# Performance work log

Measured on AMD Instinct MI355X. Metric: run time of the kernel, lower is better.

## Reference

```python
import jax, jax.numpy as jnp
import numpy as np

N = 100000
E = 3200000
H = 16


def setup_inputs() -> dict:
    key = jax.random.key(0)
    ks = jax.random.split(key, 8)
    x = jax.random.normal(ks[0], (N, 1), dtype=jnp.float32)
    edge_index = jax.random.randint(ks[1], (2, E), 0, N, dtype=jnp.int64)
    # GCNConv weights (PyG: lin has no bias by default? it has bias=True via separate bias param)
    W1 = jax.random.normal(ks[2], (1, H), dtype=jnp.float32) / np.sqrt(1.0)
    b1 = jnp.zeros((H,), dtype=jnp.float32)
    W2 = jax.random.normal(ks[3], (H, H), dtype=jnp.float32) / np.sqrt(H)
    b2 = jnp.zeros((H,), dtype=jnp.float32)
    Wf = jax.random.normal(ks[4], (H, 1), dtype=jnp.float32) / np.sqrt(H)
    bf = jnp.zeros((1,), dtype=jnp.float32)
    return {"x": x, "edge_index": edge_index, "W1": W1, "b1": b1,
            "W2": W2, "b2": b2, "Wf": Wf, "bf": bf}


def _gcn_norm(edge_index, num_nodes):
    # add self-loops, compute symmetric normalization coeffs per edge
    loops = jnp.arange(num_nodes, dtype=edge_index.dtype)
    src = jnp.concatenate([edge_index[0], loops])
    dst = jnp.concatenate([edge_index[1], loops])
    deg = jax.ops.segment_sum(jnp.ones_like(dst, dtype=jnp.float32), dst,
                              num_segments=num_nodes)
    dinv = jnp.where(deg > 0, jax.lax.rsqrt(deg), 0.0)
    norm = dinv[src] * dinv[dst]  # [E+N]
    return src, dst, norm


def _gcn_conv(h, src, dst, norm, W, b, num_nodes):
    h = h @ W                              # [N, out]
    msg = h[src] * norm[:, None]           # gather + scale, [E+N, out]
    agg = jax.ops.segment_sum(msg, dst, num_segments=num_nodes)
    return agg + b


def reference(x, edge_index, W1, b1, W2, b2, Wf, bf):
    num_nodes = x.shape[0]
    src, dst, norm = _gcn_norm(edge_index, num_nodes)
    h = _gcn_conv(x, src, dst, norm, W1, b1, num_nodes)
    h = jax.nn.relu(h)
    h = _gcn_conv(h, src, dst, norm, W2, b2, num_nodes)
    h = jax.nn.relu(h)
    out = jnp.tanh(h @ Wf + bf)            # [N, 1]
    return out
```

## Files before the change

### kernel.cpp

```cpp
#include <hip/hip_runtime.h>
#include <hip/hip_fp16.h>
#include <math.h>

#define HID 16
typedef unsigned int uint;

#define PSHIFT 7
#define PSIZE  128
#define PMASK  127
#define SRCBITS 17
#define SRCMASK 0x1FFFFu
#define SENT 0xFFFFFFFFu
#define PAD 16
#define TILE 8192
#define MAXNB 1024
#define AGT 1024
#define CAP 6144


__global__ void p_bcount(const int* __restrict__ dstA, uint* __restrict__ tileHist,
                         int e, int nb) {
    __shared__ uint hist[MAXNB];
    int t = threadIdx.x;
    for (int i = t; i < nb; i += 256) hist[i] = 0;
    __syncthreads();
    int base = blockIdx.x * TILE;
    int lim = min(TILE, e - base);
    const int4* d4 = (const int4*)(dstA + base);
    int n4 = lim >> 2;
    for (int k = t; k < n4; k += 256) {
        int4 d = d4[k];
        atomicAdd(&hist[((uint)d.x) >> PSHIFT], 1u);
        atomicAdd(&hist[((uint)d.y) >> PSHIFT], 1u);
        atomicAdd(&hist[((uint)d.z) >> PSHIFT], 1u);
        atomicAdd(&hist[((uint)d.w) >> PSHIFT], 1u);
    }
    for (int i = (n4 << 2) + t; i < lim; i += 256)
        atomicAdd(&hist[((uint)dstA[base + i]) >> PSHIFT], 1u);
    __syncthreads();
    size_t row = (size_t)blockIdx.x * nb;
    for (int i = t; i < nb; i += 256)
        tileHist[row + i] = hist[i];
}

__global__ void p_colsum(const uint* __restrict__ tileHist, uint* __restrict__ bCnt,
                         int tiles, int nb) {
    __shared__ uint red[256];
    int b = blockIdx.x;
    int t = threadIdx.x;
    uint s = 0;
    for (int ti = t; ti < tiles; ti += 256)
        s += tileHist[(size_t)ti * nb + b];
    red[t] = s;
    __syncthreads();
    for (int off = 128; off >= 1; off >>= 1) {
        if (t < off) red[t] += red[t + off];
        __syncthreads();
    }
    if (t == 0) bCnt[b] = red[0];
}

__global__ void p_bscan(const uint* __restrict__ bCnt, uint* __restrict__ cursorPad,
                        uint* __restrict__ bBase, int nb) {
    __shared__ uint tsum[256];
    int t = threadIdx.x;
    uint loc[4]; uint s = 0;
#pragma unroll
    for (int k = 0; k < 4; ++k) {
        int i = t * 4 + k;
        uint c = (i < nb) ? bCnt[i] : 0u;
        loc[k] = s; s += c;
    }
    tsum[t] = s;
    __syncthreads();
    for (int off = 1; off < 256; off <<= 1) {
        uint v = (t >= off) ? tsum[t - off] : 0u;
        __syncthreads();
        tsum[t] += v;
        __syncthreads();
    }
    uint excl = (t == 0) ? 0u : tsum[t - 1];
#pragma unroll
    for (int k = 0; k < 4; ++k) {
        int i = t * 4 + k;
        if (i < nb) {
            uint b = excl + loc[k];
            bBase[i] = b;
            cursorPad[i * PAD] = b;
        }
    }
}

__global__ void p_part(const int* __restrict__ srcA, const int* __restrict__ dstA,
                       uint* __restrict__ cursorPad, const uint* __restrict__ tileHist,
                       uint* __restrict__ part, int e, int nb) {
    __shared__ uint payload[TILE];
    __shared__ uint hist[MAXNB];
    __shared__ uint binStart[MAXNB];
    __shared__ uint cursorL[MAXNB];
    __shared__ uint gdelta[MAXNB];
    __shared__ uint tsum[256];
    int t = threadIdx.x;
    size_t row = (size_t)blockIdx.x * nb;
    for (int i = t; i < nb; i += 256) hist[i] = tileHist[row + i];
    __syncthreads();
    int base = blockIdx.x * TILE;
    int lim = min(TILE, e - base);
    const int4* s4 = (const int4*)(srcA + base);
    const int4* d4 = (const int4*)(dstA + base);
    int n4 = lim >> 2;
    uint loc[4]; uint s = 0;
#pragma unroll
    for (int k = 0; k < 4; ++k) {
        int i = t * 4 + k;
        uint c = (i < nb) ? hist[i] : 0u;
        loc[k] = s; s += c;
    }
    tsum[t] = s;
    __syncthreads();
    for (int off = 1; off < 256; off <<= 1) {
        uint v = (t >= off) ? tsum[t - off] : 0u;
        __syncthreads();
        tsum[t] += v;
        __syncthreads();
    }
    uint excl = (t == 0) ? 0u : tsum[t - 1];
#pragma unroll
    for (int k = 0; k < 4; ++k) {
        int i = t * 4 + k;
        if (i < nb) {
            uint bs = excl + loc[k];
            binStart[i] = bs; cursorL[i] = bs;
            uint c = hist[i];
            if (c) gdelta[i] = atomicAdd(&cursorPad[i * PAD], c) - bs;
        }
    }
    __syncthreads();
    for (int k = t; k < n4; k += 256) {
        int4 dd = d4[k]; int4 ss = s4[k];
#pragma unroll
        for (int q = 0; q < 4; ++q) {
            uint d = (uint)((q == 0) ? dd.x : (q == 1) ? dd.y : (q == 2) ? dd.z : dd.w);
            uint sv = (uint)((q == 0) ? ss.x : (q == 1) ? ss.y : (q == 2) ? ss.z : ss.w);
            uint w = ((d & PMASK) << SRCBITS) | sv;
            uint pos = atomicAdd(&cursorL[d >> PSHIFT], 1u);
            payload[pos] = w;
        }
    }
    for (int i = (n4 << 2) + t; i < lim; i += 256) {
        uint d = (uint)dstA[base + i];
        uint w = ((d & PMASK) << SRCBITS) | (uint)srcA[base + i];
        uint pos = atomicAdd(&cursorL[d >> PSHIFT], 1u);
        payload[pos] = w;
    }
    __syncthreads();
    int grp = t >> 4, lane16 = t & 15;
    for (int bk = grp; bk < nb; bk += 16) {
        uint c = hist[bk];
        if (!c) continue;
        uint st = binStart[bk];
        uint gd = gdelta[bk];
        for (uint i = lane16; i < c; i += 16)
            part[gd + st + i] = payload[st + i];
    }
}

__global__ __launch_bounds__(AGT)
void p_sort(uint* __restrict__ part, const uint* __restrict__ bBase,
            const uint* __restrict__ bCnt, const float* __restrict__ x,
            uint* __restrict__ rowEnd, uint* __restrict__ oversz,
            float* __restrict__ dinv, float* __restrict__ y, int n) {
    __shared__ uint lds[2 * CAP];
    __shared__ uint hist[PSIZE];
    __shared__ uint cursor[PSIZE];
    int b = blockIdx.x, t = threadIdx.x;
    uint base = bBase[b], cnt = bCnt[b];
    if (t < PSIZE) hist[t] = 0;
    if (t == 0) oversz[b] = (cnt > 2 * CAP) ? 1u : 0u;
    __syncthreads();
    bool fits = (cnt <= 2 * CAP);
    if (fits) {
        for (uint i = t; i < cnt; i += AGT) {
            uint w = part[base + i];
            lds[i] = w;
            atomicAdd(&hist[w >> SRCBITS], 1u);
        }
    } else {
        for (uint i = t; i < cnt; i += AGT)
            atomicAdd(&hist[part[base + i] >> SRCBITS], 1u);
    }
    __syncthreads();
    uint myc = (t < PSIZE) ? hist[t] : 0u;
    for (int off = 1; off < PSIZE; off <<= 1) {
        uint v = 0;
        if (t < PSIZE && t >= off) v = hist[t - off];
        __syncthreads();
        if (t < PSIZE) hist[t] += v;
        __syncthreads();
    }
    if (t < PSIZE) cursor[t] = hist[t] - myc;
    __syncthreads();
    if (fits) {
        if (cnt <= CAP) {
            for (uint i = t; i < cnt; i += AGT) {
                uint w = lds[i];
                uint pos = atomicAdd(&cursor[w >> SRCBITS], 1u);
                lds[CAP + pos] = w & SRCMASK;
            }
            __syncthreads();
            for (uint i = t; i < cnt; i += AGT)
                part[base + i] = lds[CAP + i];
        } else {
            for (uint i = t; i < cnt; i += AGT) {
                uint w = lds[i];
                uint pos = atomicAdd(&cursor[w >> SRCBITS], 1u);
                part[base + pos] = w & SRCMASK;
            }
        }
    }
    if (t < PSIZE) {
        int node = b * PSIZE + t;
        if (node < n) {
            rowEnd[node] = fits ? (base + hist[t]) : SENT;
            float d = rsqrtf((float)(myc + 1u));
            dinv[node] = d;
            y[node] = x[node] * d;
        }
    }
}

__global__ void p_g1mlp(const uint* __restrict__ part, const uint* __restrict__ rowEnd,
                        const uint* __restrict__ bBase,
                        const float* __restrict__ y, const float* __restrict__ dinv,
                        const float* __restrict__ W1, const float* __restrict__ b1,
                        const float* __restrict__ W2,
                        __half* __restrict__ g, int n) {
    int i = blockIdx.x * blockDim.x + threadIdx.x;
    if (i >= n) return;
    uint en = rowEnd[i];
    if (en == SENT) return;
    uint st = (i & PMASK) ? rowEnd[i - 1] : bBase[i >> PSHIFT];
    float tsum = 0.0f;
    uint e = st;
    for (; e + 4 <= en; e += 4)
        tsum += y[part[e]] + y[part[e + 1]] + y[part[e + 2]] + y[part[e + 3]];
    for (; e < en; ++e) tsum += y[part[e]];
    float d = dinv[i];
    float sv = d * (tsum + y[i]);
    float h1[HID], h2[HID];
#pragma unroll
    for (int j = 0; j < HID; ++j)
        h1[j] = fmaxf(sv * W1[j] + b1[j], 0.0f);
#pragma unroll
    for (int k = 0; k < HID; ++k) {
        float a = 0.0f;
#pragma unroll
        for (int j = 0; j < HID; ++j)
            a = fmaf(h1[j], W2[j * HID + k], a);
        h2[k] = a * d;
    }
    __half2 hh[8];
#pragma unroll
    for (int q = 0; q < 8; ++q)
        hh[q] = __floats2half2_rn(h2[2 * q], h2[2 * q + 1]);
    uint4* gp = (uint4*)(g + (size_t)i * HID);
    gp[0] = *reinterpret_cast<uint4*>(&hh[0]);
    gp[1] = *reinterpret_cast<uint4*>(&hh[4]);
}

__global__ void p_g2out(const uint* __restrict__ part, const uint* __restrict__ rowEnd,
                        const uint* __restrict__ bBase,
                        const __half* __restrict__ g, const float* __restrict__ dinv,
                        const float* __restrict__ b2, const float* __restrict__ Wf,
                        const float* __restrict__ bf,
                        float* __restrict__ out, int n) {
    int gid = blockIdx.x * blockDim.x + threadIdx.x;
    int node = gid >> 3, lane = gid & 7;
    if (node >= n) return;
    uint en = rowEnd[node];
    if (en == SENT) return;
    uint st = (node & PMASK) ? rowEnd[node - 1] : bBase[node >> PSHIFT];
    const __half2* gh = (const __half2*)g;
    float ax = 0.0f, ay = 0.0f;
    uint e = st;
    for (; e + 4 <= en; e += 4) {
        uint s0 = part[e], s1 = part[e + 1], s2 = part[e + 2], s3 = part[e + 3];
        float2 f0 = __half22float2(gh[(size_t)s0 * 8 + lane]);
        float2 f1 = __half22float2(gh[(size_t)s1 * 8 + lane]);
        float2 f2 = __half22float2(gh[(size_t)s2 * 8 + lane]);
        float2 f3 = __half22float2(gh[(size_t)s3 * 8 + lane]);
        ax += (f0.x + f1.x) + (f2.x + f3.x);
        ay += (f0.y + f1.y) + (f2.y + f3.y);
    }
    for (; e < en; ++e) {
        float2 f = __half22float2(gh[(size_t)part[e] * 8 + lane]);
        ax += f.x; ay += f.y;
    }
    float2 fs = __half22float2(gh[(size_t)node * 8 + lane]);
    ax += fs.x; ay += fs.y;
    float d = dinv[node];
    int j0 = 2 * lane, j1 = 2 * lane + 1;
    float h0 = fmaxf(fmaf(d, ax, b2[j0]), 0.0f);
    float h1 = fmaxf(fmaf(d, ay, b2[j1]), 0.0f);
    float v = h0 * Wf[j0] + h1 * Wf[j1];
#pragma unroll
    for (int m = 4; m >= 1; m >>= 1)
        v += __shfl_xor(v, m, 8);
    if (lane == 0) out[node] = tanhf(v + bf[0]);
}

__global__ __launch_bounds__(AGT)
void p_slow1(const uint* __restrict__ part, const uint* __restrict__ bBase,
             const uint* __restrict__ bCnt, const uint* __restrict__ oversz,
             const float* __restrict__ y, const float* __restrict__ dinv,
             const float* __restrict__ W1, const float* __restrict__ b1,
             const float* __restrict__ W2, __half* __restrict__ g, int n) {
    int b = blockIdx.x;
    if (!oversz[b]) return;
    __shared__ float acc[PSIZE];
    int t = threadIdx.x;
    if (t < PSIZE) acc[t] = 0.0f;
    __syncthreads();
    uint base = bBase[b], cnt = bCnt[b];
    for (uint i = base + t; i < base + cnt; i += AGT) {
        uint w = part[i];
        atomicAdd(&acc[w >> SRCBITS], y[w & SRCMASK]);
    }
    __syncthreads();
    if (t < PSIZE) {
        int node = b * PSIZE + t;
        if (node < n) {
            float d = dinv[node];
            float sv = d * (acc[t] + y[node]);
            float h1[HID], h2[HID];
#pragma unroll
            for (int j = 0; j < HID; ++j)
                h1[j] = fmaxf(sv * W1[j] + b1[j], 0.0f);
#pragma unroll
            for (int k = 0; k < HID; ++k) {
                float a = 0.0f;
#pragma unroll
                for (int j = 0; j < HID; ++j)
                    a = fmaf(h1[j], W2[j * HID + k], a);
                h2[k] = a * d;
            }
            __half2 hh[8];
#pragma unroll
            for (int q = 0; q < 8; ++q)
                hh[q] = __floats2half2_rn(h2[2 * q], h2[2 * q + 1]);
            uint4* gp = (uint4*)(g + (size_t)node * HID);
            gp[0] = *reinterpret_cast<uint4*>(&hh[0]);
            gp[1] = *reinterpret_cast<uint4*>(&hh[4]);
        }
    }
}

__global__ __launch_bounds__(AGT)
void p_slow2(const uint* __restrict__ part, const uint* __restrict__ bBase,
             const uint* __restrict__ bCnt, const uint* __restrict__ oversz,
             const __half* __restrict__ g, const float* __restrict__ dinv,
             const float* __restrict__ b2, const float* __restrict__ Wf,
             const float* __restrict__ bf, float* __restrict__ out, int n) {
    int b = blockIdx.x;
    if (!oversz[b]) return;
    __shared__ float acc[PSIZE][HID + 1];
    int t = threadIdx.x;
    const __half2* gh = (const __half2*)g;
    {
        int r = t >> 3, q = t & 7;
        int node = b * PSIZE + r;
        float2 f = make_float2(0.0f, 0.0f);
        if (node < n) f = __half22float2(gh[(size_t)node * 8 + q]);
        acc[r][2 * q] = f.x; acc[r][2 * q + 1] = f.y;
    }
    __syncthreads();
    uint base = bBase[b], cnt = bCnt[b];
    int gi = t >> 3, sub = t & 7;
    for (uint i = base + gi; i < base + cnt; i += AGT / 8) {
        uint w = part[i];
        uint src = w & SRCMASK;
        uint dl = w >> SRCBITS;
        float2 f = __half22float2(gh[(size_t)src * 8 + sub]);
        atomicAdd(&acc[dl][2 * sub], f.x);
        atomicAdd(&acc[dl][2 * sub + 1], f.y);
    }
    __syncthreads();
    if (t < PSIZE) {
        int node = b * PSIZE + t;
        if (node < n) {
            float d = dinv[node];
            float o = bf[0];
#pragma unroll
            for (int j = 0; j < HID; ++j) {
                float h = fmaxf(fmaf(d, acc[t][j], b2[j]), 0.0f);
                o = fmaf(h, Wf[j], o);
            }
            out[node] = tanhf(o);
        }
    }
}


__global__ void f_init_deg(float* deg, int n) {
    int i = blockIdx.x * blockDim.x + threadIdx.x;
    if (i < n) deg[i] = 1.0f;
}

__global__ void f_deg_accum(const int* __restrict__ dstA, float* deg, int e) {
    int i = blockIdx.x * blockDim.x + threadIdx.x;
    if (i < e) atomicAdd(&deg[dstA[i]], 1.0f);
}

__global__ void f_dinv_s(const float* __restrict__ x, float* deg_dinv, float* s, int n) {
    int i = blockIdx.x * blockDim.x + threadIdx.x;
    if (i < n) {
        float d = rsqrtf(deg_dinv[i]);
        deg_dinv[i] = d;
        s[i] = x[i] * d * d;
    }
}

__global__ void f_s_edge(const int* __restrict__ srcA, const int* __restrict__ dstA,
                         const float* __restrict__ x, const float* __restrict__ dinv,
                         float* s, int e) {
    int i = blockIdx.x * blockDim.x + threadIdx.x;
    if (i < e) {
        int si = srcA[i], di = dstA[i];
        atomicAdd(&s[di], x[si] * dinv[si] * dinv[di]);
    }
}

__global__ void f_node_mlp(const float* __restrict__ s, const float* __restrict__ dinv,
                           const float* __restrict__ W1, const float* __restrict__ b1,
                           const float* __restrict__ W2,
                           float* __restrict__ h2pre, float* __restrict__ agg2, int n) {
    int i = blockIdx.x * blockDim.x + threadIdx.x;
    if (i >= n) return;
    float sv = s[i];
    float h1[HID];
#pragma unroll
    for (int j = 0; j < HID; ++j)
        h1[j] = fmaxf(sv * W1[j] + b1[j], 0.0f);
    float d2 = dinv[i] * dinv[i];
    float h2[HID];
#pragma unroll
    for (int k = 0; k < HID; ++k) {
        float acc = 0.0f;
#pragma unroll
        for (int j = 0; j < HID; ++j)
            acc = fmaf(h1[j], W2[j * HID + k], acc);
        h2[k] = acc;
    }
    float4* hp = (float4*)(h2pre + (size_t)i * HID);
    float4* ap = (float4*)(agg2 + (size_t)i * HID);
#pragma unroll
    for (int q = 0; q < 4; ++q) {
        float4 v = make_float4(h2[q*4+0], h2[q*4+1], h2[q*4+2], h2[q*4+3]);
        hp[q] = v;
        ap[q] = make_float4(v.x * d2, v.y * d2, v.z * d2, v.w * d2);
    }
}

__global__ void f_agg_edge(const int* __restrict__ srcA, const int* __restrict__ dstA,
                           const float* __restrict__ dinv,
                           const float* __restrict__ h2pre,
                           float* __restrict__ agg2, int e) {
    int gid = blockIdx.x * blockDim.x + threadIdx.x;
    int ei = gid >> 4;
    int j  = gid & 15;
    if (ei < e) {
        int si = srcA[ei], di = dstA[ei];
        float w = dinv[si] * dinv[di];
        atomicAdd(&agg2[(size_t)di * HID + j], h2pre[(size_t)si * HID + j] * w);
    }
}

__global__ void f_out(const float* __restrict__ agg2, const float* __restrict__ b2,
                      const float* __restrict__ Wf, const float* __restrict__ bf,
                      float* __restrict__ out, int n) {
    int i = blockIdx.x * blockDim.x + threadIdx.x;
    if (i >= n) return;
    float acc = bf[0];
#pragma unroll
    for (int k = 0; k < HID; ++k) {
        float h = fmaxf(agg2[(size_t)i * HID + k] + b2[k], 0.0f);
        acc = fmaf(h, Wf[k], acc);
    }
    out[i] = tanhf(acc);
}


extern "C" void kernel_launch(void* const* d_in, const int* in_sizes, int n_in,
                              void* d_out, int out_size, void* d_ws, size_t ws_size,
                              hipStream_t stream) {
    const float* x  = (const float*)d_in[0];
    const int*   ei = (const int*)d_in[1];
    const float* W1 = (const float*)d_in[2];
    const float* b1 = (const float*)d_in[3];
    const float* W2 = (const float*)d_in[4];
    const float* b2 = (const float*)d_in[5];
    const float* Wf = (const float*)d_in[6];
    const float* bf = (const float*)d_in[7];
    float* out = (float*)d_out;

    const int N = in_sizes[0];
    const int E = in_sizes[1] / 2;
    const int* srcA = ei;
    const int* dstA = ei + E;
    (void)n_in; (void)out_size;

    const int NB = (N + PMASK) >> PSHIFT;
    const int B = 256;
    int nb_n = (N + B - 1) / B;
    int nb_e = (E + B - 1) / B;
    int tiles = (E + TILE - 1) / TILE;

    size_t off = 0;
    auto takeo = [&](size_t bytes) -> size_t {
        size_t p = off;
        off = (off + bytes + 255) & ~(size_t)255;
        return p;
    };
    size_t o_curp = takeo((size_t)NB * PAD * 4);
    size_t o_bb   = takeo((size_t)NB * 4);
    size_t o_bc   = takeo((size_t)NB * 4);
    size_t o_ovs  = takeo((size_t)NB * 4);
    size_t o_dinv = takeo((size_t)N * 4);
    size_t o_y    = takeo((size_t)N * 4);
    size_t o_re   = takeo((size_t)N * 4);
    size_t o_th   = takeo((size_t)tiles * NB * 4);
    size_t o_part = takeo((size_t)E * 4);
    size_t o_g    = takeo((size_t)N * HID * 2);
    size_t need = off;

    if (N <= (1 << SRCBITS) && NB <= MAXNB && ws_size >= need) {
        char* ws = (char*)d_ws;
        uint*  cursorPad = (uint*)(ws + o_curp);
        uint*  bBase     = (uint*)(ws + o_bb);
        uint*  bCnt      = (uint*)(ws + o_bc);
        uint*  oversz    = (uint*)(ws + o_ovs);
        float* dinv      = (float*)(ws + o_dinv);
        float* y         = (float*)(ws + o_y);
        uint*  rowEnd    = (uint*)(ws + o_re);
        uint*  tileHist  = (uint*)(ws + o_th);
        uint*  part      = (uint*)(ws + o_part);
        __half* g        = (__half*)(ws + o_g);

        int nb_g2 = (int)(((size_t)N * 8 + B - 1) / B);

        hipLaunchKernelGGL(p_bcount, dim3(tiles), dim3(B), 0, stream, dstA, tileHist, E, NB);
        hipLaunchKernelGGL(p_colsum, dim3(NB), dim3(B), 0, stream, tileHist, bCnt, tiles, NB);
        hipLaunchKernelGGL(p_bscan,  dim3(1), dim3(B), 0, stream, bCnt, cursorPad, bBase, NB);
        hipLaunchKernelGGL(p_part,   dim3(tiles), dim3(B), 0, stream, srcA, dstA, cursorPad, tileHist, part, E, NB);
        hipLaunchKernelGGL(p_sort,   dim3(NB), dim3(AGT), 0, stream,
                           part, bBase, bCnt, x, rowEnd, oversz, dinv, y, N);
        hipLaunchKernelGGL(p_g1mlp,  dim3(nb_n), dim3(B), 0, stream,
                           part, rowEnd, bBase, y, dinv, W1, b1, W2, g, N);
        hipLaunchKernelGGL(p_slow1,  dim3(NB), dim3(AGT), 0, stream,
                           part, bBase, bCnt, oversz, y, dinv, W1, b1, W2, g, N);
        hipLaunchKernelGGL(p_g2out,  dim3(nb_g2), dim3(B), 0, stream,
                           part, rowEnd, bBase, g, dinv, b2, Wf, bf, out, N);
        hipLaunchKernelGGL(p_slow2,  dim3(NB), dim3(AGT), 0, stream,
                           part, bBase, bCnt, oversz, g, dinv, b2, Wf, bf, out, N);
    } else {
        size_t foff = 0;
        auto ftake = [&](size_t bytes) -> size_t {
            size_t p = foff;
            foff = (foff + bytes + 255) & ~(size_t)255;
            return p;
        };
        char* ws = (char*)d_ws;
        float* dinv  = (float*)(ws + ftake((size_t)N * 4));
        float* s     = (float*)(ws + ftake((size_t)N * 4));
        float* h2pre = (float*)(ws + ftake((size_t)N * HID * 4));
        float* agg2  = (float*)(ws + ftake((size_t)N * HID * 4));

        long long totD = (long long)E * HID;
        int nb_d = (int)((totD + B - 1) / B);

        hipLaunchKernelGGL(f_init_deg,  dim3(nb_n), dim3(B), 0, stream, dinv, N);
        hipLaunchKernelGGL(f_deg_accum, dim3(nb_e), dim3(B), 0, stream, dstA, dinv, E);
        hipLaunchKernelGGL(f_dinv_s,    dim3(nb_n), dim3(B), 0, stream, x, dinv, s, N);
        hipLaunchKernelGGL(f_s_edge,    dim3(nb_e), dim3(B), 0, stream, srcA, dstA, x, dinv, s, E);
        hipLaunchKernelGGL(f_node_mlp,  dim3(nb_n), dim3(B), 0, stream,
                           s, dinv, W1, b1, W2, h2pre, agg2, N);
        hipLaunchKernelGGL(f_agg_edge,  dim3(nb_d), dim3(B), 0, stream,
                           srcA, dstA, dinv, h2pre, agg2, E);
        hipLaunchKernelGGL(f_out,       dim3(nb_n), dim3(B), 0, stream,
                           agg2, b2, Wf, bf, out, N);
    }
}
```

Before: 116.6 us.

## Widen g2 gathers to 16-byte loads, resize partition and fallback blocks

p_g2out now gives each node 2 lanes instead of 8, and each lane loads a full uint4 (8 halves) per neighbour, which cuts the number of gather instructions and removes most of the shuffle reduction. p_part moves to 512-thread blocks with a matching scan, to get more parallelism in the scatter. The oversize fallback kernels p_slow1/p_slow2 drop to 256 threads, and p_slow2's initial load becomes a loop. The trade-off is fewer threads in flight to hide the random-gather latency in p_g2out, and higher register pressure from the eight accumulators per lane.

```diff
diff --git a/kernel.cpp b/kernel.cpp
--- a/kernel.cpp
+++ b/kernel.cpp
@@ -15,6 +15,8 @@
 #define TILE 8192
 #define MAXNB 1024
 #define AGT 1024
+#define SLT 256
+#define PBT 512
 #define CAP 6144
 
 
@@ -91,34 +93,35 @@
     }
 }
 
-__global__ void p_part(const int* __restrict__ srcA, const int* __restrict__ dstA,
-                       uint* __restrict__ cursorPad, const uint* __restrict__ tileHist,
-                       uint* __restrict__ part, int e, int nb) {
+__global__ __launch_bounds__(PBT)
+void p_part(const int* __restrict__ srcA, const int* __restrict__ dstA,
+            uint* __restrict__ cursorPad, const uint* __restrict__ tileHist,
+            uint* __restrict__ part, int e, int nb) {
     __shared__ uint payload[TILE];
     __shared__ uint hist[MAXNB];
     __shared__ uint binStart[MAXNB];
     __shared__ uint cursorL[MAXNB];
     __shared__ uint gdelta[MAXNB];
-    __shared__ uint tsum[256];
+    __shared__ uint tsum[PBT];
     int t = threadIdx.x;
     size_t row = (size_t)blockIdx.x * nb;
-    for (int i = t; i < nb; i += 256) hist[i] = tileHist[row + i];
+    for (int i = t; i < nb; i += PBT) hist[i] = tileHist[row + i];
     __syncthreads();
     int base = blockIdx.x * TILE;
     int lim = min(TILE, e - base);
     const int4* s4 = (const int4*)(srcA + base);
     const int4* d4 = (const int4*)(dstA + base);
     int n4 = lim >> 2;
-    uint loc[4]; uint s = 0;
-#pragma unroll
-    for (int k = 0; k < 4; ++k) {
-        int i = t * 4 + k;
+    uint loc[2]; uint s = 0;
+#pragma unroll
+    for (int k = 0; k < 2; ++k) {
+        int i = t * 2 + k;
         uint c = (i < nb) ? hist[i] : 0u;
         loc[k] = s; s += c;
     }
     tsum[t] = s;
     __syncthreads();
-    for (int off = 1; off < 256; off <<= 1) {
+    for (int off = 1; off < PBT; off <<= 1) {
         uint v = (t >= off) ? tsum[t - off] : 0u;
         __syncthreads();
         tsum[t] += v;
@@ -126,8 +129,8 @@
     }
     uint excl = (t == 0) ? 0u : tsum[t - 1];
 #pragma unroll
-    for (int k = 0; k < 4; ++k) {
-        int i = t * 4 + k;
+    for (int k = 0; k < 2; ++k) {
+        int i = t * 2 + k;
         if (i < nb) {
             uint bs = excl + loc[k];
             binStart[i] = bs; cursorL[i] = bs;
@@ -136,7 +139,7 @@
         }
     }
     __syncthreads();
-    for (int k = t; k < n4; k += 256) {
+    for (int k = t; k < n4; k += PBT) {
         int4 dd = d4[k]; int4 ss = s4[k];
 #pragma unroll
         for (int q = 0; q < 4; ++q) {
@@ -147,7 +150,7 @@
             payload[pos] = w;
         }
     }
-    for (int i = (n4 << 2) + t; i < lim; i += 256) {
+    for (int i = (n4 << 2) + t; i < lim; i += PBT) {
         uint d = (uint)dstA[base + i];
         uint w = ((d & PMASK) << SRCBITS) | (uint)srcA[base + i];
         uint pos = atomicAdd(&cursorL[d >> PSHIFT], 1u);
@@ -155,7 +158,7 @@
     }
     __syncthreads();
     int grp = t >> 4, lane16 = t & 15;
-    for (int bk = grp; bk < nb; bk += 16) {
+    for (int bk = grp; bk < nb; bk += PBT / 16) {
         uint c = hist[bk];
         if (!c) continue;
         uint st = binStart[bk];
@@ -268,6 +271,15 @@
     gp[1] = *reinterpret_cast<uint4*>(&hh[4]);
 }
 
+#define ACC8(v)                                                         \
+    {                                                                   \
+        float2 f_;                                                      \
+        f_ = __half22float2(*(const __half2*)&(v).x); a0.x += f_.x; a0.y += f_.y; \
+        f_ = __half22float2(*(const __half2*)&(v).y); a1.x += f_.x; a1.y += f_.y; \
+        f_ = __half22float2(*(const __half2*)&(v).z); a2.x += f_.x; a2.y += f_.y; \
+        f_ = __half22float2(*(const __half2*)&(v).w); a3.x += f_.x; a3.y += f_.y; \
+    }
+
 __global__ void p_g2out(const uint* __restrict__ part, const uint* __restrict__ rowEnd,
                         const uint* __restrict__ bBase,
                         const __half* __restrict__ g, const float* __restrict__ dinv,
@@ -275,41 +287,49 @@
                         const float* __restrict__ bf,
                         float* __restrict__ out, int n) {
     int gid = blockIdx.x * blockDim.x + threadIdx.x;
-    int node = gid >> 3, lane = gid & 7;
+    int node = gid >> 1, lane = gid & 1;
     if (node >= n) return;
     uint en = rowEnd[node];
     if (en == SENT) return;
     uint st = (node & PMASK) ? rowEnd[node - 1] : bBase[node >> PSHIFT];
-    const __half2* gh = (const __half2*)g;
-    float ax = 0.0f, ay = 0.0f;
+    const uint4* gq = (const uint4*)g;
+    float2 a0 = make_float2(0.f, 0.f), a1 = a0, a2 = a0, a3 = a0;
     uint e = st;
     for (; e + 4 <= en; e += 4) {
         uint s0 = part[e], s1 = part[e + 1], s2 = part[e + 2], s3 = part[e + 3];
-        float2 f0 = __half22float2(gh[(size_t)s0 * 8 + lane]);
-        float2 f1 = __half22float2(gh[(size_t)s1 * 8 + lane]);
-        float2 f2 = __half22float2(gh[(size_t)s2 * 8 + lane]);
-        float2 f3 = __half22float2(gh[(size_t)s3 * 8 + lane]);
-        ax += (f0.x + f1.x) + (f2.x + f3.x);
-        ay += (f0.y + f1.y) + (f2.y + f3.y);
+        uint4 v0 = gq[(size_t)s0 * 2 + lane];
+        uint4 v1 = gq[(size_t)s1 * 2 + lane];
+        uint4 v2 = gq[(size_t)s2 * 2 + lane];
+        uint4 v3 = gq[(size_t)s3 * 2 + lane];
+        ACC8(v0); ACC8(v1); ACC8(v2); ACC8(v3);
     }
     for (; e < en; ++e) {
-        float2 f = __half22float2(gh[(size_t)part[e] * 8 + lane]);
-        ax += f.x; ay += f.y;
-    }
-    float2 fs = __half22float2(gh[(size_t)node * 8 + lane]);
-    ax += fs.x; ay += fs.y;
+        uint4 v = gq[(size_t)part[e] * 2 + lane];
+        ACC8(v);
+    }
+    {
+        uint4 v = gq[(size_t)node * 2 + lane];
+        ACC8(v);
+    }
     float d = dinv[node];
-    int j0 = 2 * lane, j1 = 2 * lane + 1;
-    float h0 = fmaxf(fmaf(d, ax, b2[j0]), 0.0f);
-    float h1 = fmaxf(fmaf(d, ay, b2[j1]), 0.0f);
-    float v = h0 * Wf[j0] + h1 * Wf[j1];
-#pragma unroll
-    for (int m = 4; m >= 1; m >>= 1)
-        v += __shfl_xor(v, m, 8);
-    if (lane == 0) out[node] = tanhf(v + bf[0]);
-}
-
-__global__ __launch_bounds__(AGT)
+    int jb = lane * 8;
+    float vsum = 0.0f;
+    {
+        float h;
+        h = fmaxf(fmaf(d, a0.x, b2[jb + 0]), 0.0f); vsum = fmaf(h, Wf[jb + 0], vsum);
+        h = fmaxf(fmaf(d, a0.y, b2[jb + 1]), 0.0f); vsum = fmaf(h, Wf[jb + 1], vsum);
+        h = fmaxf(fmaf(d, a1.x, b2[jb + 2]), 0.0f); vsum = fmaf(h, Wf[jb + 2], vsum);
+        h = fmaxf(fmaf(d, a1.y, b2[jb + 3]), 0.0f); vsum = fmaf(h, Wf[jb + 3], vsum);
+        h = fmaxf(fmaf(d, a2.x, b2[jb + 4]), 0.0f); vsum = fmaf(h, Wf[jb + 4], vsum);
+        h = fmaxf(fmaf(d, a2.y, b2[jb + 5]), 0.0f); vsum = fmaf(h, Wf[jb + 5], vsum);
+        h = fmaxf(fmaf(d, a3.x, b2[jb + 6]), 0.0f); vsum = fmaf(h, Wf[jb + 6], vsum);
+        h = fmaxf(fmaf(d, a3.y, b2[jb + 7]), 0.0f); vsum = fmaf(h, Wf[jb + 7], vsum);
+    }
+    vsum += __shfl_xor(vsum, 1, 2);
+    if (lane == 0) out[node] = tanhf(vsum + bf[0]);
+}
+
+__global__ __launch_bounds__(SLT)
 void p_slow1(const uint* __restrict__ part, const uint* __restrict__ bBase,
              const uint* __restrict__ bCnt, const uint* __restrict__ oversz,
              const float* __restrict__ y, const float* __restrict__ dinv,
@@ -322,7 +342,7 @@
     if (t < PSIZE) acc[t] = 0.0f;
     __syncthreads();
     uint base = bBase[b], cnt = bCnt[b];
-    for (uint i = base + t; i < base + cnt; i += AGT) {
+    for (uint i = base + t; i < base + cnt; i += SLT) {
         uint w = part[i];
         atomicAdd(&acc[w >> SRCBITS], y[w & SRCMASK]);
     }
@@ -355,7 +375,7 @@
     }
 }
 
-__global__ __launch_bounds__(AGT)
+__global__ __launch_bounds__(SLT)
 void p_slow2(const uint* __restrict__ part, const uint* __restrict__ bBase,
              const uint* __restrict__ bCnt, const uint* __restrict__ oversz,
              const __half* __restrict__ g, const float* __restrict__ dinv,
@@ -366,8 +386,8 @@
     __shared__ float acc[PSIZE][HID + 1];
     int t = threadIdx.x;
     const __half2* gh = (const __half2*)g;
-    {
-        int r = t >> 3, q = t & 7;
+    for (int r = t >> 3; r < PSIZE; r += SLT / 8) {
+        int q = t & 7;
         int node = b * PSIZE + r;
         float2 f = make_float2(0.0f, 0.0f);
         if (node < n) f = __half22float2(gh[(size_t)node * 8 + q]);
@@ -376,7 +396,7 @@
     __syncthreads();
     uint base = bBase[b], cnt = bCnt[b];
     int gi = t >> 3, sub = t & 7;
-    for (uint i = base + gi; i < base + cnt; i += AGT / 8) {
+    for (uint i = base + gi; i < base + cnt; i += SLT / 8) {
         uint w = part[i];
         uint src = w & SRCMASK;
         uint dl = w >> SRCBITS;
@@ -546,21 +566,21 @@
         uint*  part      = (uint*)(ws + o_part);
         __half* g        = (__half*)(ws + o_g);
 
-        int nb_g2 = (int)(((size_t)N * 8 + B - 1) / B);
+        int nb_g2 = (int)(((size_t)N * 2 + B - 1) / B);
 
         hipLaunchKernelGGL(p_bcount, dim3(tiles), dim3(B), 0, stream, dstA, tileHist, E, NB);
         hipLaunchKernelGGL(p_colsum, dim3(NB), dim3(B), 0, stream, tileHist, bCnt, tiles, NB);
         hipLaunchKernelGGL(p_bscan,  dim3(1), dim3(B), 0, stream, bCnt, cursorPad, bBase, NB);
-        hipLaunchKernelGGL(p_part,   dim3(tiles), dim3(B), 0, stream, srcA, dstA, cursorPad, tileHist, part, E, NB);
+        hipLaunchKernelGGL(p_part,   dim3(tiles), dim3(PBT), 0, stream, srcA, dstA, cursorPad, tileHist, part, E, NB);
         hipLaunchKernelGGL(p_sort,   dim3(NB), dim3(AGT), 0, stream,
                            part, bBase, bCnt, x, rowEnd, oversz, dinv, y, N);
         hipLaunchKernelGGL(p_g1mlp,  dim3(nb_n), dim3(B), 0, stream,
                            part, rowEnd, bBase, y, dinv, W1, b1, W2, g, N);
-        hipLaunchKernelGGL(p_slow1,  dim3(NB), dim3(AGT), 0, stream,
+        hipLaunchKernelGGL(p_slow1,  dim3(NB), dim3(SLT), 0, stream,
                            part, bBase, bCnt, oversz, y, dinv, W1, b1, W2, g, N);
         hipLaunchKernelGGL(p_g2out,  dim3(nb_g2), dim3(B), 0, stream,
                            part, rowEnd, bBase, g, dinv, b2, Wf, bf, out, N);
-        hipLaunchKernelGGL(p_slow2,  dim3(NB), dim3(AGT), 0, stream,
+        hipLaunchKernelGGL(p_slow2,  dim3(NB), dim3(SLT), 0, stream,
                            part, bBase, bCnt, oversz, g, dinv, b2, Wf, bf, out, N);
     } else {
         size_t foff = 0;
```

Measured after the change: 117.6 us. No clear change (+0.9%).
